# Performance work log

Measured on AMD Instinct MI355X. Metric: run time of the kernel, lower is better.

The kernel has to match this reference:

```python
import jax, jax.numpy as jnp
import numpy as np

B, T, V, D, C, d, TSZ, L, P = 8, 12, 512, 1, 128, 8, 3, 3, 12
BETA = TSZ - 1


def _gauss(emb, mu, isg):
    # Gaussian_component: sum over d of -0.5*(emb-mu)^2 * inv_sigma^2
    return jnp.sum(-0.5 * (emb - mu) ** 2 * isg ** 2, axis=-1)


def _gfs(h, fw, fb, gw, gb):
    # GFS: Conv2d(T->C, kernel (1,C)) over x[B,T,V,C] -> [B,C,V], then 1x1 GLU
    s = jnp.einsum('btvc,otc->bov', h, fw) + fb[None, :, None]
    g = jnp.einsum('bov,po->bpv', s, gw) + gb[None, :, None]
    lhs, rhs = jnp.split(g, 2, axis=1)
    return lhs * jax.nn.sigmoid(rhs)  # B,C,V


def _forward(x, sape, tape, srpe, trpe, zeros_x, zeros_tape, range_mask,
             input_w, input_b, fs0_fc_w, fs0_fc_b, fs0_glu_w, fs0_glu_b,
             mus, inv_sigmas, xproj_w, xproj_b, seproj_w, teproj_w, ln_g, ln_b,
             fs_fc_w, fs_fc_b, fs_glu_w, fs_glu_b, glu_w, glu_b, out_w, out_b):
    h = x @ input_w + input_b  # B,T,V,C (InputLayer)
    tape_pad = jnp.concatenate([zeros_tape, tape], axis=1)  # B,T+beta,1,d
    mask = range_mask.reshape(V, TSZ, V)  # [j, k, i]
    skips = [_gfs(h, fs0_fc_w, fs0_fc_b, fs0_glu_w, fs0_glu_b)]
    for l in range(L):
        h_pad = jnp.concatenate([zeros_x, h], axis=1)  # B,T+beta,V,C
        # all T shifted windows at once (vectorizes the per-timestep loop)
        xwin = jnp.stack([h_pad[:, k:k + T] for k in range(TSZ)], axis=2)     # B,T,k,V,C
        twin = jnp.stack([tape_pad[:, k:k + T] for k in range(TSZ)], axis=2)  # B,T,k,1,d
        mu, isg = mus[l], inv_sigmas[l]
        gi = _gauss(sape, mu[0], isg[0])              # (V,)   source node i
        gj = _gauss(sape, mu[1], isg[1])              # (V,)   target node j
        gti = _gauss(tape, mu[2], isg[2])[:, :, 0]    # (B,T)  tape_i
        gtj = _gauss(twin, mu[3], isg[3])[..., 0]     # (B,T,k) tape_j windows
        ge = _gauss(srpe, mu[4], isg[4])              # (V,V)  [i,j]
        gtr = _gauss(trpe, mu[5], isg[5])[:, 0]       # (k,)
        # log S[b,t,j,k,i]; original gaussian[b,k,i,j] -> reshape -> transpose gives S[b,j,(k,i)]
        logS = (gi[None, None, None, None, :] + gj[None, None, :, None, None]
                + gti[:, :, None, None, None] + gtj[:, :, None, :, None]
                + ge.T[None, None, :, None, :] + gtr[None, None, None, :, None])
        S = jnp.exp(logS) * mask[None, None]          # B,T,V(j),k,V(i)
        # STPGConv: bmm(S, x) over the (k,i) axis
        agg = jnp.einsum('btjki,btkic->btjc', S, xwin)  # B,T,V,C
        z = agg @ xproj_w[l] + xproj_b[l]               # B,T,V,2C
        z = z + sape @ seproj_w[l] + tape @ teproj_w[l]  # SE:(V,2C); TE:(B,T,1,2C) broadcasts over V
        mn = jnp.mean(z, axis=-1, keepdims=True)
        var = jnp.mean((z - mn) ** 2, axis=-1, keepdims=True)
        z = (z - mn) * jax.lax.rsqrt(var + 1e-5) * ln_g[l] + ln_b[l]
        lhs, rhs = jnp.split(z, 2, axis=-1)
        h = lhs * jax.nn.sigmoid(rhs)                   # B,T,V,C
        skips.append(_gfs(h, fs_fc_w[l], fs_fc_b[l], fs_glu_w[l], fs_glu_b[l]))
    hc = jnp.concatenate(skips, axis=1)                 # B,(L+1)*C,V
    g = jnp.einsum('bov,po->bpv', hc, glu_w) + glu_b[None, :, None]
    lhs, rhs = jnp.split(g, 2, axis=1)
    gated = lhs * jax.nn.sigmoid(rhs)                   # B,4C,V
    out = jnp.einsum('bov,po->bpv', gated, out_w) + out_b[None, :, None]  # B,P*D,V
    return out[:, :, :, None]                           # D==1 -> (B,P,V,1)


def setup_inputs() -> dict:
    key = jax.random.key(0)

    def nrm(i, shape, s=1.0):
        return s * jax.random.normal(jax.random.fold_in(key, i), shape, dtype=jnp.float32)

    inp = {
        'x': nrm(0, (B, T, V, D)),
        'sape': nrm(1, (V, d), 0.5),
        'tape': nrm(2, (B, T, 1, d), 0.5),
        'srpe': nrm(3, (V, V, d), 0.5),
        'trpe': nrm(4, (TSZ, 1, d), 0.5),
        'zeros_x': jnp.zeros((B, BETA, V, C), jnp.float32),
        'zeros_tape': jnp.zeros((B, BETA, 1, d), jnp.float32),
        'range_mask': (jax.random.uniform(jax.random.fold_in(key, 5), (V, TSZ * V)) < 0.7).astype(jnp.float32),
        'input_w': nrm(6, (D, C), 0.5),
        'input_b': jnp.zeros((C,), jnp.float32),
        'fs0_fc_w': nrm(7, (C, T, C), 1.0 / np.sqrt(T * C)),
        'fs0_fc_b': jnp.zeros((C,), jnp.float32),
        'fs0_glu_w': nrm(8, (2 * C, C), 1.0 / np.sqrt(C)),
        'fs0_glu_b': jnp.zeros((2 * C,), jnp.float32),
        'mus': nrm(9, (L, 6, d)),
        'inv_sigmas': nrm(10, (L, 6, d), 0.3),
        'xproj_w': nrm(11, (L, C, 2 * C), 1.0 / np.sqrt(C)),
        'xproj_b': jnp.zeros((L, 2 * C), jnp.float32),
        'seproj_w': nrm(12, (L, d, 2 * C), 1.0 / np.sqrt(d)),
        'teproj_w': nrm(13, (L, d, 2 * C), 1.0 / np.sqrt(d)),
        'ln_g': jnp.ones((L, 2 * C), jnp.float32),
        'ln_b': jnp.zeros((L, 2 * C), jnp.float32),
        'fs_fc_w': nrm(14, (L, C, T, C), 1.0 / np.sqrt(T * C)),
        'fs_fc_b': jnp.zeros((L, C), jnp.float32),
        'fs_glu_w': nrm(15, (L, 2 * C, C), 1.0 / np.sqrt(C)),
        'fs_glu_b': jnp.zeros((L, 2 * C), jnp.float32),
        'glu_w': nrm(16, (8 * C, 4 * C), 1.0 / np.sqrt(4 * C)),
        'glu_b': jnp.zeros((8 * C,), jnp.float32),
        'out_w': nrm(17, (P * D, 4 * C), 1.0 / np.sqrt(4 * C)),
        'out_b': jnp.zeros((P * D,), jnp.float32),
    }
    return inp


def reference(x, sape, tape, srpe, trpe, zeros_x, zeros_tape, range_mask,
              input_w, input_b, fs0_fc_w, fs0_fc_b, fs0_glu_w, fs0_glu_b,
              mus, inv_sigmas, xproj_w, xproj_b, seproj_w, teproj_w, ln_g, ln_b,
              fs_fc_w, fs_fc_b, fs_glu_w, fs_glu_b, glu_w, glu_b, out_w, out_b):
    return _forward(x, sape, tape, srpe, trpe, zeros_x, zeros_tape, range_mask,
                    input_w, input_b, fs0_fc_w, fs0_fc_b, fs0_glu_w, fs0_glu_b,
                    mus, inv_sigmas, xproj_w, xproj_b, seproj_w, teproj_w, ln_g, ln_b,
                    fs_fc_w, fs_fc_b, fs_glu_w, fs_glu_b, glu_w, glu_b, out_w, out_b)
```

## Files before the change

kernel.cpp:

```cpp
#include <hip/hip_runtime.h>
#include <cstddef>


#define BB 8
#define TT 12
#define VV 512
#define CC 128

typedef unsigned short ushort_t;
typedef float f32x4 __attribute__((ext_vector_type(4)));
typedef short bf16x8 __attribute__((ext_vector_type(8)));

__device__ __forceinline__ float sigmoidf_(float x){ return 1.0f/(1.0f+expf(-x)); }

__device__ __forceinline__ void split_bf16(float x, ushort_t& hi, ushort_t& lo){
  unsigned u = __float_as_uint(x);
  hi = (ushort_t)(u >> 16);
  float r = x - __uint_as_float(u & 0xFFFF0000u);
  lo = (ushort_t)(__float_as_uint(r) >> 16);
}

__device__ __forceinline__ float gauss8(const float* __restrict__ e,
                                        const float* __restrict__ mu,
                                        const float* __restrict__ sg){
  float a = 0.f;
  #pragma unroll
  for (int dd=0; dd<8; ++dd){
    float df = e[dd]-mu[dd];
    float s  = sg[dd];
    a = fmaf(-0.5f*df*df, s*s, a);
  }
  return a;
}

__global__ __launch_bounds__(256) void k_prep(
    const float* __restrict__ fs0_fc_w, const float* __restrict__ fs_fc_w,
    const float* __restrict__ fs0_glu_w, const float* __restrict__ fs_glu_w,
    const float* __restrict__ glu_w, const float* __restrict__ out_w,
    float* __restrict__ fwT, float* __restrict__ gwT,
    float* __restrict__ gluT, float* __restrict__ outT){
  int job = blockIdx.y;
  int gid = blockIdx.x*256 + threadIdx.x;
  if (job < 4){
    if (gid >= 196608) return;
    const float* src = (job==0) ? fs0_fc_w : fs_fc_w + (size_t)(job-1)*196608;
    float* dst = fwT + (size_t)job*196608;
    int r = gid / 1536, c = gid % 1536;
    dst[(size_t)c*128 + r] = src[gid];
  } else if (job < 8){
    if (gid >= 32768) return;
    int sl = job-4;
    const float* src = (sl==0) ? fs0_glu_w : fs_glu_w + (size_t)(sl-1)*32768;
    float* dst = gwT + (size_t)sl*32768;
    int r = gid / 128, c = gid % 128;
    dst[(size_t)c*256 + r] = src[gid];
  } else if (job == 8){
    if (gid >= 524288) return;
    int r = gid / 512, c = gid % 512;
    gluT[(size_t)c*1024 + r] = glu_w[gid];
  } else {
    if (gid >= 6144) return;
    int r = gid / 512, c = gid % 512;
    outT[(size_t)c*12 + r] = out_w[gid];
  }
}

__global__ __launch_bounds__(256) void k_input(const float* __restrict__ x,
    const float* __restrict__ iw, const float* __restrict__ ib,
    float* __restrict__ hA, ushort_t* __restrict__ hhiT, ushort_t* __restrict__ hloT){
  int bt = blockIdx.x;
  int v0 = blockIdx.y*64;
  int c = threadIdx.x >> 1, half = threadIdx.x & 1;
  int vb = v0 + half*32;
  float wc = iw[c], bc = ib[c];
  const float* xp = x + (size_t)bt*VV + vb;
  float hv[32];
  #pragma unroll
  for (int u=0;u<32;++u) hv[u] = fmaf(xp[u], wc, bc);
  #pragma unroll
  for (int u=0;u<32;++u) hA[((size_t)bt*VV + vb + u)*CC + c] = hv[u];
  unsigned wh[16], wl[16];
  #pragma unroll
  for (int m=0;m<16;++m){
    ushort_t h0,l0,h1,l1;
    split_bf16(hv[2*m],   h0, l0);
    split_bf16(hv[2*m+1], h1, l1);
    wh[m] = (unsigned)h0 | ((unsigned)h1<<16);
    wl[m] = (unsigned)l0 | ((unsigned)l1<<16);
  }
  ushort_t* hp = hhiT + ((size_t)bt*CC + c)*VV + vb;
  ushort_t* lp = hloT + ((size_t)bt*CC + c)*VV + vb;
  #pragma unroll
  for (int q=0;q<4;++q){
    *(uint4*)(hp + q*8) = make_uint4(wh[q*4],wh[q*4+1],wh[q*4+2],wh[q*4+3]);
    *(uint4*)(lp + q*8) = make_uint4(wl[q*4],wl[q*4+1],wl[q*4+2],wl[q*4+3]);
  }
}

__global__ __launch_bounds__(256) void k_gfs1(const float* __restrict__ h,
    const float* __restrict__ fwT, float* __restrict__ s_part){
  int vt = blockIdx.x, b = blockIdx.y, ts = blockIdx.z;
  int tid = threadIdx.x;
  int v0 = vt*32;
  __shared__ float hT[32][34];
  int vtt = tid & 3, ot = tid >> 2;
  float acc[2][8];
  #pragma unroll
  for (int a=0;a<2;++a)
    #pragma unroll
    for (int u=0;u<8;++u) acc[a][u] = 0.f;

  for (int tt=0; tt<3; ++tt){
    int t = ts*3 + tt;
    const float* hbase = h + ((size_t)(b*TT+t)*VV)*CC;
    for (int cch=0; cch<4; ++cch){
      int c0 = cch*32;
      __syncthreads();
      { int vv = tid>>3, c4 = tid&7;
        float4 val = *(const float4*)(hbase + (size_t)(v0+vv)*CC + c0 + c4*4);
        hT[c4*4+0][vv]=val.x; hT[c4*4+1][vv]=val.y;
        hT[c4*4+2][vv]=val.z; hT[c4*4+3][vv]=val.w; }
      __syncthreads();
      const float* fwb = fwT + ((size_t)t*128 + c0)*128 + ot*2;
      for (int c=0;c<32;++c){
        float2 wv = *(const float2*)(fwb + (size_t)c*128);
        float hv[8];
        *(float4*)hv     = *(const float4*)&hT[c][vtt*8];
        *(float4*)(hv+4) = *(const float4*)&hT[c][vtt*8+4];
        #pragma unroll
        for (int u=0;u<8;++u){
          acc[0][u] = fmaf(wv.x, hv[u], acc[0][u]);
          acc[1][u] = fmaf(wv.y, hv[u], acc[1][u]);
        }
      }
    }
  }
  float* sp = s_part + (((size_t)ts*BB+b)*128 + ot*2)*VV + v0 + vtt*8;
  #pragma unroll
  for (int a=0;a<2;++a){
    *(float4*)(sp + (size_t)a*VV)     = *(float4*)&acc[a][0];
    *(float4*)(sp + (size_t)a*VV + 4) = *(float4*)&acc[a][4];
  }
}

__global__ __launch_bounds__(256) void k_gfs2(const float* __restrict__ s_part,
    const float* __restrict__ fb, const float* __restrict__ gwT,
    const float* __restrict__ gb, float* __restrict__ hc, int slot){
  int vt = blockIdx.x, b = blockIdx.y;
  int v0 = vt*32; int tid = threadIdx.x;
  __shared__ float sL[128][36];
  for (int u=0;u<16;++u){
    int lid = u*256 + tid; int o = lid>>5, vv = lid&31;
    float sum = fb[o];
    #pragma unroll
    for (int sp=0;sp<4;++sp)
      sum += s_part[(((size_t)sp*BB+b)*128 + o)*VV + v0 + vv];
    sL[o][vv] = sum;
  }
  __syncthreads();
  int oo = tid & 127, vg = tid >> 7;
  float accL[16], accR[16];
  #pragma unroll
  for (int u=0;u<16;++u){ accL[u]=0.f; accR[u]=0.f; }
  for (int op=0; op<128; ++op){
    float glv = gwT[(size_t)op*256 + oo];
    float grv = gwT[(size_t)op*256 + 128 + oo];
    float sv[16];
    #pragma unroll
    for (int q=0;q<4;++q) *(float4*)(sv+q*4) = *(const float4*)&sL[op][vg*16 + q*4];
    #pragma unroll
    for (int u=0;u<16;++u){ accL[u]=fmaf(glv,sv[u],accL[u]); accR[u]=fmaf(grv,sv[u],accR[u]); }
  }
  float bl = gb[oo], br = gb[128+oo];
  float outv[16];
  #pragma unroll
  for (int u=0;u<16;++u) outv[u] = (accL[u]+bl)*sigmoidf_(accR[u]+br);
  float* dst = hc + ((size_t)b*512 + slot*128 + oo)*VV + v0 + vg*16;
  #pragma unroll
  for (int q=0;q<4;++q) *(float4*)(dst+q*4) = *(float4*)(outv+q*4);
}

__global__ void k_smalls(const float* __restrict__ sape, const float* __restrict__ tape,
    const float* __restrict__ trpe, const float* __restrict__ mus,
    const float* __restrict__ isgs, int l,
    float* __restrict__ gi, float* __restrict__ gj,
    float* __restrict__ E, float* __restrict__ F, float* __restrict__ gtr){
  int tid = threadIdx.x;
  const float* mu = mus  + (size_t)l*48;
  const float* sg = isgs + (size_t)l*48;
  if (tid < 512){
    const float* e = sape + (size_t)tid*8;
    gi[tid] = gauss8(e, mu+0,  sg+0);
    gj[tid] = gauss8(e, mu+8,  sg+8);
  }
  if (tid < 96)
    E[tid] = expf(gauss8(tape + (size_t)tid*8, mu+16, sg+16));
  if (tid < 288){
    int k = tid % 3, bt = tid / 3;
    int t = bt % TT, b = bt / TT;
    int s = t + k - 2;
    F[tid] = (s >= 0) ? expf(gauss8(tape + (size_t)(b*TT+s)*8, mu+24, sg+24)) : 0.f;
  }
  if (tid < 3)
    gtr[tid] = gauss8(trpe + (size_t)tid*8, mu+40, sg+40);
}

__global__ __launch_bounds__(256) void k_W(const float* __restrict__ srpe,
    const float* __restrict__ mask, const float* __restrict__ mus,
    const float* __restrict__ isgs, int l,
    const float* __restrict__ gi, const float* __restrict__ gj,
    const float* __restrict__ gtr,
    ushort_t* __restrict__ Whi, ushort_t* __restrict__ Wlo){
  int it = blockIdx.x, jt = blockIdx.y;
  int tid = threadIdx.x;
  int ii = tid & 15, jj = tid >> 4;
  int i = it*16 + ii, j = jt*16 + jj;
  const float* mu = mus  + (size_t)l*48 + 32;
  const float* sg = isgs + (size_t)l*48 + 32;
  float ge = gauss8(srpe + ((size_t)i*VV + j)*8, mu, sg);
  float base = gi[i] + gj[j] + ge;
  float gk[3] = {gtr[0], gtr[1], gtr[2]};
  __shared__ unsigned tile[16][17];
  int arr = tid>>7, rem = tid&127, jr = rem>>3, p = rem&7;
  for (int k=0;k<3;++k){
    float m = mask[(size_t)j*1536 + k*512 + i];
    float val = m * expf(base + gk[k]);
    ushort_t hi, lo; split_bf16(val, hi, lo);
    __syncthreads();
    tile[jj][ii] = (unsigned)hi | ((unsigned)lo<<16);
    __syncthreads();
    unsigned w0 = tile[jr][2*p], w1 = tile[jr][2*p+1];
    unsigned outw = (arr==0) ? ((w0&0xFFFFu) | (w1<<16))
                             : ((w0>>16) | (w1&0xFFFF0000u));
    ushort_t* dst = (arr ? Wlo : Whi) + ((size_t)k*VV + jt*16 + jr)*VV + it*16 + 2*p;
    *(unsigned*)dst = outw;
  }
}

__global__ __launch_bounds__(256) void k_stpg(
    const ushort_t* __restrict__ hhiT, const ushort_t* __restrict__ hloT,
    const ushort_t* __restrict__ Whi,  const ushort_t* __restrict__ Wlo,
    const float* __restrict__ E, const float* __restrict__ F,
    float* __restrict__ agg){
  int bt = blockIdx.x; int b = bt/TT, t = bt - b*TT;
  int j0 = blockIdx.y * 128;
  int tid = threadIdx.x;
  int lane = tid & 63, wid = tid >> 6;
  int jw = (wid>>1)*64, cw = (wid&1)*64;

  __shared__ ushort_t Ahi_s[128*40];
  __shared__ ushort_t Alo_s[128*40];
  __shared__ ushort_t Bhi_s[128*40];
  __shared__ ushort_t Blo_s[128*40];

  f32x4 acc[4][4];
  #pragma unroll
  for (int a=0;a<4;++a)
    #pragma unroll
    for (int u=0;u<4;++u) acc[a][u] = (f32x4){0.f,0.f,0.f,0.f};

  int kmin = (t>=2) ? 0 : (2-t);
  float Fk[3] = {F[bt*3+0], F[bt*3+1], F[bt*3+2]};
  float Eb = E[bt];

  int ro = (lane&15)*40 + (lane>>4)*8;

  for (int k=kmin; k<3; ++k){
    int s = t + k - 2;
    const ushort_t* gAhi = Whi  + ((size_t)k*VV + j0)*VV;
    const ushort_t* gAlo = Wlo  + ((size_t)k*VV + j0)*VV;
    const ushort_t* gBhi = hhiT + (size_t)(b*TT+s)*CC*VV;
    const ushort_t* gBlo = hloT + (size_t)(b*TT+s)*CC*VV;
    for (int i0=0; i0<512; i0+=32){
      __syncthreads();
      #pragma unroll
      for (int p=0;p<2;++p){
        int sl = p*256 + tid;
        int r = sl>>2, q = sl&3;
        size_t go = (size_t)r*VV + i0 + q*8;
        int lo_ = r*40 + q*8;
        *(uint4*)&Ahi_s[lo_] = *(const uint4*)(gAhi + go);
        *(uint4*)&Alo_s[lo_] = *(const uint4*)(gAlo + go);
        *(uint4*)&Bhi_s[lo_] = *(const uint4*)(gBhi + go);
        *(uint4*)&Blo_s[lo_] = *(const uint4*)(gBlo + go);
      }
      __syncthreads();
      bf16x8 ah[4], al[4], bh[4], bl[4];
      #pragma unroll
      for (int f=0; f<4; ++f){
        ah[f] = *(const bf16x8*)&Ahi_s[(jw + f*16)*40 + ro];
        al[f] = *(const bf16x8*)&Alo_s[(jw + f*16)*40 + ro];
        bh[f] = *(const bf16x8*)&Bhi_s[(cw + f*16)*40 + ro];
        bl[f] = *(const bf16x8*)&Blo_s[(cw + f*16)*40 + ro];
      }
      #pragma unroll
      for (int jf=0;jf<4;++jf)
        #pragma unroll
        for (int cf=0;cf<4;++cf){
          acc[jf][cf] = __builtin_amdgcn_mfma_f32_16x16x32_bf16(ah[jf], bh[cf], acc[jf][cf],0,0,0);
          acc[jf][cf] = __builtin_amdgcn_mfma_f32_16x16x32_bf16(ah[jf], bl[cf], acc[jf][cf],0,0,0);
          acc[jf][cf] = __builtin_amdgcn_mfma_f32_16x16x32_bf16(al[jf], bh[cf], acc[jf][cf],0,0,0);
        }
    }
    if (k < 2){
      float r = Fk[k]/Fk[k+1];
      #pragma unroll
      for (int jf=0;jf<4;++jf)
        #pragma unroll
        for (int cf=0;cf<4;++cf) acc[jf][cf] *= r;
    }
  }
  float fin = Fk[2]*Eb;
  #pragma unroll
  for (int jf=0;jf<4;++jf){
    #pragma unroll
    for (int cf=0;cf<4;++cf){
      int row = j0 + jw + jf*16 + (lane>>4)*4;
      int col = cw + cf*16 + (lane&15);
      float* dst = agg + ((size_t)bt*VV + row)*CC + col;
      #pragma unroll
      for (int e=0;e<4;++e) dst[(size_t)e*CC] = acc[jf][cf][e]*fin;
    }
  }
}

__global__ __launch_bounds__(256) void k_xln(float* __restrict__ hB,
    const float* __restrict__ xw, const float* __restrict__ xb,
    const float* __restrict__ sw, const float* __restrict__ tw,
    const float* __restrict__ sape, const float* __restrict__ tape,
    const float* __restrict__ lng, const float* __restrict__ lnb, int l,
    ushort_t* __restrict__ hhiT, ushort_t* __restrict__ hloT){
  int v0 = blockIdx.x * 8;
  int bt = blockIdx.y;
  int tid = threadIdx.x;
  __shared__ float aL[8][128];
  __shared__ float se[8][8];
  __shared__ float te[8];
  __shared__ float zL[8][260];
  __shared__ float stat[8][2];
  float* hrow = hB + ((size_t)bt*VV + v0)*CC;
  { int vv = tid>>5, cc4 = tid&31;
    *(float4*)&aL[vv][cc4*4] = *(const float4*)(hrow + (size_t)vv*CC + cc4*4); }
  if (tid < 64) se[tid>>3][tid&7] = sape[(size_t)(v0 + (tid>>3))*8 + (tid&7)];
  if (tid >= 64 && tid < 72) te[tid-64] = tape[(size_t)bt*8 + (tid-64)];
  __syncthreads();

  const float* xwl = xw + (size_t)l*32768;
  const float* swl = sw + (size_t)l*2048;
  const float* twl = tw + (size_t)l*2048;
  float common = xb[l*256 + tid];
  #pragma unroll
  for (int dd=0; dd<8; ++dd) common = fmaf(te[dd], twl[dd*256+tid], common);
  float z[8];
  #pragma unroll
  for (int vv=0; vv<8; ++vv){
    float sacc = common;
    #pragma unroll
    for (int dd=0; dd<8; ++dd) sacc = fmaf(se[vv][dd], swl[dd*256+tid], sacc);
    z[vv] = sacc;
  }
  for (int c4=0; c4<32; ++c4){
    float x0 = xwl[(c4*4+0)*256 + tid];
    float x1 = xwl[(c4*4+1)*256 + tid];
    float x2 = xwl[(c4*4+2)*256 + tid];
    float x3 = xwl[(c4*4+3)*256 + tid];
    #pragma unroll
    for (int vv=0; vv<8; ++vv){
      float4 a4 = *(const float4*)&aL[vv][c4*4];
      z[vv] = fmaf(a4.x,x0, fmaf(a4.y,x1, fmaf(a4.z,x2, fmaf(a4.w,x3, z[vv]))));
    }
  }
  #pragma unroll
  for (int vv=0; vv<8; ++vv) zL[vv][tid] = z[vv];
  __syncthreads();
  { int vv = tid>>5, sub = tid&31;
    float s1=0.f, s2=0.f;
    #pragma unroll
    for (int u=0; u<8; ++u){ float val = zL[vv][sub + u*32]; s1 += val; s2 = fmaf(val,val,s2); }
    #pragma unroll
    for (int off=16; off>=1; off>>=1){
      s1 += __shfl_down(s1, off, 32);
      s2 += __shfl_down(s2, off, 32);
    }
    if (sub==0){
      float mn = s1*(1.f/256.f);
      float var = s2*(1.f/256.f) - mn*mn;
      stat[vv][0] = mn;
      stat[vv][1] = 1.f/sqrtf(var + 1e-5f);
    }
  }
  __syncthreads();
  { int vv = tid>>5, sub = tid&31;
    float mn = stat[vv][0], rs = stat[vv][1];
    float4 zl = *(const float4*)&zL[vv][sub*4];
    float4 zr = *(const float4*)&zL[vv][sub*4+128];
    float zlv[4] = {zl.x,zl.y,zl.z,zl.w};
    float zrv[4] = {zr.x,zr.y,zr.z,zr.w};
    float ov[4];
    #pragma unroll
    for (int u=0; u<4; ++u){
      int c = sub*4 + u;
      float nl = (zlv[u]-mn)*rs*lng[l*256 + c]       + lnb[l*256 + c];
      float nr = (zrv[u]-mn)*rs*lng[l*256 + 128 + c] + lnb[l*256 + 128 + c];
      ov[u] = nl * sigmoidf_(nr);
    }
    *(float4*)(hrow + (size_t)vv*CC + sub*4) = *(float4*)ov;
    zL[vv][sub*4+0]=ov[0]; zL[vv][sub*4+1]=ov[1]; zL[vv][sub*4+2]=ov[2]; zL[vv][sub*4+3]=ov[3];
  }
  __syncthreads();
  { int cc = tid & 127, sel = tid >> 7;
    float g[8];
    #pragma unroll
    for (int u=0;u<8;++u) g[u] = zL[u][cc];
    unsigned w[4];
    #pragma unroll
    for (int m=0;m<4;++m){
      ushort_t h0,l0,h1,l1;
      split_bf16(g[2*m],   h0, l0);
      split_bf16(g[2*m+1], h1, l1);
      w[m] = sel ? ((unsigned)l0 | ((unsigned)l1<<16))
                 : ((unsigned)h0 | ((unsigned)h1<<16));
    }
    ushort_t* dst = (sel ? hloT : hhiT) + ((size_t)bt*CC + cc)*VV + v0;
    *(uint4*)dst = make_uint4(w[0],w[1],w[2],w[3]);
  }
}

__global__ __launch_bounds__(256) void k_final(const float* __restrict__ hc,
    const float* __restrict__ gluT, const float* __restrict__ glub,
    const float* __restrict__ outT, const float* __restrict__ outb,
    float* __restrict__ out){
  int b = blockIdx.y; int v0 = blockIdx.x * 8;
  int tid = threadIdx.x;
  __shared__ float hcl[512][8];
  __shared__ float gl[512][9];
  for (int u=0; u<16; ++u){
    int lid = u*256 + tid; int o = lid>>3, vv = lid&7;
    hcl[o][vv] = hc[((size_t)b*512 + o)*VV + v0 + vv];
  }
  __syncthreads();
  float aL0[8], aR0[8], aL1[8], aR1[8];
  #pragma unroll
  for (int u=0;u<8;++u){ aL0[u]=0.f; aR0[u]=0.f; aL1[u]=0.f; aR1[u]=0.f; }
  for (int o=0; o<512; ++o){
    const float* grow = gluT + (size_t)o*1024;
    float g0 = grow[tid], g1 = grow[tid+256], g2 = grow[tid+512], g3 = grow[tid+768];
    float hv[8];
    *(float4*)hv     = *(const float4*)&hcl[o][0];
    *(float4*)(hv+4) = *(const float4*)&hcl[o][4];
    #pragma unroll
    for (int u=0;u<8;++u){
      aL0[u]=fmaf(g0,hv[u],aL0[u]); aL1[u]=fmaf(g1,hv[u],aL1[u]);
      aR0[u]=fmaf(g2,hv[u],aR0[u]); aR1[u]=fmaf(g3,hv[u],aR1[u]);
    }
  }
  float bL0 = glub[tid], bL1 = glub[tid+256], bR0 = glub[tid+512], bR1 = glub[tid+768];
  #pragma unroll
  for (int u=0;u<8;++u){
    gl[tid][u]     = (aL0[u]+bL0)*sigmoidf_(aR0[u]+bR0);
    gl[tid+256][u] = (aL1[u]+bL1)*sigmoidf_(aR1[u]+bR1);
  }
  __syncthreads();
  if (tid < 96){
    int r = tid>>3, vv = tid&7;
    float acc = outb[r];
    for (int q=0; q<512; ++q) acc = fmaf(outT[(size_t)q*12 + r], gl[q][vv], acc);
    out[(size_t)b*6144 + r*512 + v0 + vv] = acc;
  }
}

extern "C" void kernel_launch(void* const* d_in, const int* in_sizes, int n_in,
                              void* d_out, int out_size, void* d_ws, size_t ws_size,
                              hipStream_t stream){
  const float* x        = (const float*)d_in[0];
  const float* sape     = (const float*)d_in[1];
  const float* tape     = (const float*)d_in[2];
  const float* srpe     = (const float*)d_in[3];
  const float* trpe     = (const float*)d_in[4];
  const float* mask     = (const float*)d_in[7];
  const float* input_w  = (const float*)d_in[8];
  const float* input_b  = (const float*)d_in[9];
  const float* fs0_fc_w = (const float*)d_in[10];
  const float* fs0_fc_b = (const float*)d_in[11];
  const float* fs0_glu_w= (const float*)d_in[12];
  const float* fs0_glu_b= (const float*)d_in[13];
  const float* mus      = (const float*)d_in[14];
  const float* isg      = (const float*)d_in[15];
  const float* xproj_w  = (const float*)d_in[16];
  const float* xproj_b  = (const float*)d_in[17];
  const float* seproj_w = (const float*)d_in[18];
  const float* teproj_w = (const float*)d_in[19];
  const float* ln_g     = (const float*)d_in[20];
  const float* ln_b     = (const float*)d_in[21];
  const float* fs_fc_w  = (const float*)d_in[22];
  const float* fs_fc_b  = (const float*)d_in[23];
  const float* fs_glu_w = (const float*)d_in[24];
  const float* fs_glu_b = (const float*)d_in[25];
  const float* glu_w    = (const float*)d_in[26];
  const float* glu_b    = (const float*)d_in[27];
  const float* out_w    = (const float*)d_in[28];
  const float* out_b    = (const float*)d_in[29];

  float* ws    = (float*)d_ws;
  float* hA    = ws;
  float* hc    = hA    + 6291456;
  float* s_part= hc    + 2097152;
  float* fwT   = s_part+ 2097152;
  float* gwT   = fwT   + 786432;
  float* gluT  = gwT   + 131072;
  float* outT  = gluT  + 524288;
  float* gi    = outT  + 6144;
  float* gj    = gi    + 512;
  float* Ebuf  = gj    + 512;
  float* Fbuf  = Ebuf  + 96;
  float* gtr   = Fbuf  + 288;
  ushort_t* hhiT = (ushort_t*)(gtr + 16);
  ushort_t* hloT = hhiT + 6291456;
  ushort_t* Whi  = hloT + 6291456;
  ushort_t* Wlo  = Whi  + 786432;

  k_prep<<<dim3(2048,10),256,0,stream>>>(fs0_fc_w, fs_fc_w, fs0_glu_w, fs_glu_w,
                                         glu_w, out_w, fwT, gwT, gluT, outT);
  k_input<<<dim3(96,8),256,0,stream>>>(x, input_w, input_b, hA, hhiT, hloT);
  k_gfs1<<<dim3(16,8,4),256,0,stream>>>(hA, fwT, s_part);
  k_gfs2<<<dim3(16,8),256,0,stream>>>(s_part, fs0_fc_b, gwT, fs0_glu_b, hc, 0);

  for (int l=0; l<3; ++l){
    k_smalls<<<1,512,0,stream>>>(sape, tape, trpe, mus, isg, l, gi, gj, Ebuf, Fbuf, gtr);
    k_W<<<dim3(32,32),256,0,stream>>>(srpe, mask, mus, isg, l, gi, gj, gtr, Whi, Wlo);
    k_stpg<<<dim3(96,4),256,0,stream>>>(hhiT, hloT, Whi, Wlo, Ebuf, Fbuf, hA);
    k_xln<<<dim3(64,96),256,0,stream>>>(hA, xproj_w, xproj_b, seproj_w, teproj_w,
                                        sape, tape, ln_g, ln_b, l, hhiT, hloT);
    k_gfs1<<<dim3(16,8,4),256,0,stream>>>(hA, fwT + (size_t)(l+1)*196608, s_part);
    k_gfs2<<<dim3(16,8),256,0,stream>>>(s_part, fs_fc_b + l*128, gwT + (size_t)(l+1)*32768,
                                        fs_glu_b + l*256, hc, l+1);
  }
  k_final<<<dim3(64,8),256,0,stream>>>(hc, gluT, glu_b, outT, out_b, (float*)d_out);
}
```

Before: 992.8 us.

## Rewrite projection+LayerNorm+GLU kernel on bf16x3 MFMA with concatenated weights

The per-layer x/spatial/temporal projection kernel, previously a scalar FP32 FMA loop over 8 nodes per block, now runs on MFMA 16x16x32 bf16 instructions with a hi/lo split (three products) to keep near-FP32 accuracy. The projection, spatial and temporal embedding weights plus the bias are packed once in the prep kernel into a single K=160 concatenated matrix. The embeddings and a constant-one column are folded into the A operand. LayerNorm statistics are reduced across lanes with shuffles, and each block now covers 128 nodes. This targets the compute-bound scalar GEMM, at the cost of heavy register use (32 accumulators) and only 384 blocks.

```diff
diff --git a/kernel.cpp b/kernel.cpp
--- a/kernel.cpp
+++ b/kernel.cpp
@@ -37,8 +37,11 @@
     const float* __restrict__ fs0_fc_w, const float* __restrict__ fs_fc_w,
     const float* __restrict__ fs0_glu_w, const float* __restrict__ fs_glu_w,
     const float* __restrict__ glu_w, const float* __restrict__ out_w,
+    const float* __restrict__ xw, const float* __restrict__ sw,
+    const float* __restrict__ tw, const float* __restrict__ xb2,
     float* __restrict__ fwT, float* __restrict__ gwT,
-    float* __restrict__ gluT, float* __restrict__ outT){
+    float* __restrict__ gluT, float* __restrict__ outT,
+    ushort_t* __restrict__ xcat_hi, ushort_t* __restrict__ xcat_lo){
   int job = blockIdx.y;
   int gid = blockIdx.x*256 + threadIdx.x;
   if (job < 4){
@@ -58,10 +61,25 @@
     if (gid >= 524288) return;
     int r = gid / 512, c = gid % 512;
     gluT[(size_t)c*1024 + r] = glu_w[gid];
-  } else {
+  } else if (job == 9){
     if (gid >= 6144) return;
     int r = gid / 512, c = gid % 512;
     outT[(size_t)c*12 + r] = out_w[gid];
+  } else {
+    if (gid >= 122880) return;
+    int ll  = gid / 40960;
+    int rem = gid - ll*40960;
+    int col = rem / 160;
+    int k   = rem - col*160;
+    float val;
+    if (k < 128)       val = xw[(size_t)ll*32768 + (size_t)k*256 + col];
+    else if (k < 136)  val = sw[(size_t)ll*2048 + (size_t)(k-128)*256 + col];
+    else if (k < 144)  val = tw[(size_t)ll*2048 + (size_t)(k-136)*256 + col];
+    else if (k == 144) val = xb2[ll*256 + col];
+    else               val = 0.f;
+    ushort_t hi, lo; split_bf16(val, hi, lo);
+    xcat_hi[gid] = hi;
+    xcat_lo[gid] = lo;
   }
 }
 
@@ -324,105 +342,127 @@
   }
 }
 
-__global__ __launch_bounds__(256) void k_xln(float* __restrict__ hB,
-    const float* __restrict__ xw, const float* __restrict__ xb,
-    const float* __restrict__ sw, const float* __restrict__ tw,
+__global__ __launch_bounds__(256,2) void k_xln2(
+    float* __restrict__ hA,
+    const ushort_t* __restrict__ xcat_hi, const ushort_t* __restrict__ xcat_lo,
     const float* __restrict__ sape, const float* __restrict__ tape,
     const float* __restrict__ lng, const float* __restrict__ lnb, int l,
     ushort_t* __restrict__ hhiT, ushort_t* __restrict__ hloT){
-  int v0 = blockIdx.x * 8;
-  int bt = blockIdx.y;
+  int vt = blockIdx.x, bt = blockIdx.y;
+  int v0 = vt*128;
   int tid = threadIdx.x;
-  __shared__ float aL[8][128];
-  __shared__ float se[8][8];
-  __shared__ float te[8];
-  __shared__ float zL[8][260];
-  __shared__ float stat[8][2];
-  float* hrow = hB + ((size_t)bt*VV + v0)*CC;
-  { int vv = tid>>5, cc4 = tid&31;
-    *(float4*)&aL[vv][cc4*4] = *(const float4*)(hrow + (size_t)vv*CC + cc4*4); }
-  if (tid < 64) se[tid>>3][tid&7] = sape[(size_t)(v0 + (tid>>3))*8 + (tid&7)];
-  if (tid >= 64 && tid < 72) te[tid-64] = tape[(size_t)bt*8 + (tid-64)];
+  int lane = tid & 63, w = tid >> 6;
+  int l15 = lane & 15, l4 = lane >> 4;
+  int ko = l4*8;
+
+  __shared__ float sef[128][8];
+  __shared__ float tef[8];
+  __shared__ float lnwS[256], lnbS[256];
+  { int r2 = tid>>1, hh = tid&1;
+    *(float4*)&sef[r2][hh*4] = *(const float4*)(sape + (size_t)(v0+r2)*8 + hh*4); }
+  if (tid < 8) tef[tid] = tape[(size_t)bt*8 + tid];
+  lnwS[tid] = lng[l*256 + tid];
+  lnbS[tid] = lnb[l*256 + tid];
   __syncthreads();
 
-  const float* xwl = xw + (size_t)l*32768;
-  const float* swl = sw + (size_t)l*2048;
-  const float* twl = tw + (size_t)l*2048;
-  float common = xb[l*256 + tid];
-  #pragma unroll
-  for (int dd=0; dd<8; ++dd) common = fmaf(te[dd], twl[dd*256+tid], common);
-  float z[8];
-  #pragma unroll
-  for (int vv=0; vv<8; ++vv){
-    float sacc = common;
-    #pragma unroll
-    for (int dd=0; dd<8; ++dd) sacc = fmaf(se[vv][dd], swl[dd*256+tid], sacc);
-    z[vv] = sacc;
-  }
-  for (int c4=0; c4<32; ++c4){
-    float x0 = xwl[(c4*4+0)*256 + tid];
-    float x1 = xwl[(c4*4+1)*256 + tid];
-    float x2 = xwl[(c4*4+2)*256 + tid];
-    float x3 = xwl[(c4*4+3)*256 + tid];
-    #pragma unroll
-    for (int vv=0; vv<8; ++vv){
-      float4 a4 = *(const float4*)&aL[vv][c4*4];
-      z[vv] = fmaf(a4.x,x0, fmaf(a4.y,x1, fmaf(a4.z,x2, fmaf(a4.w,x3, z[vv]))));
-    }
-  }
-  #pragma unroll
-  for (int vv=0; vv<8; ++vv) zL[vv][tid] = z[vv];
-  __syncthreads();
-  { int vv = tid>>5, sub = tid&31;
-    float s1=0.f, s2=0.f;
-    #pragma unroll
-    for (int u=0; u<8; ++u){ float val = zL[vv][sub + u*32]; s1 += val; s2 = fmaf(val,val,s2); }
-    #pragma unroll
-    for (int off=16; off>=1; off>>=1){
-      s1 += __shfl_down(s1, off, 32);
-      s2 += __shfl_down(s2, off, 32);
-    }
-    if (sub==0){
-      float mn = s1*(1.f/256.f);
-      float var = s2*(1.f/256.f) - mn*mn;
-      stat[vv][0] = mn;
-      stat[vv][1] = 1.f/sqrtf(var + 1e-5f);
-    }
-  }
-  __syncthreads();
-  { int vv = tid>>5, sub = tid&31;
-    float mn = stat[vv][0], rs = stat[vv][1];
-    float4 zl = *(const float4*)&zL[vv][sub*4];
-    float4 zr = *(const float4*)&zL[vv][sub*4+128];
-    float zlv[4] = {zl.x,zl.y,zl.z,zl.w};
-    float zrv[4] = {zr.x,zr.y,zr.z,zr.w};
-    float ov[4];
-    #pragma unroll
-    for (int u=0; u<4; ++u){
-      int c = sub*4 + u;
-      float nl = (zlv[u]-mn)*rs*lng[l*256 + c]       + lnb[l*256 + c];
-      float nr = (zrv[u]-mn)*rs*lng[l*256 + 128 + c] + lnb[l*256 + 128 + c];
-      ov[u] = nl * sigmoidf_(nr);
-    }
-    *(float4*)(hrow + (size_t)vv*CC + sub*4) = *(float4*)ov;
-    zL[vv][sub*4+0]=ov[0]; zL[vv][sub*4+1]=ov[1]; zL[vv][sub*4+2]=ov[2]; zL[vv][sub*4+3]=ov[3];
-  }
-  __syncthreads();
-  { int cc = tid & 127, sel = tid >> 7;
-    float g[8];
-    #pragma unroll
-    for (int u=0;u<8;++u) g[u] = zL[u][cc];
-    unsigned w[4];
-    #pragma unroll
-    for (int m=0;m<4;++m){
-      ushort_t h0,l0,h1,l1;
-      split_bf16(g[2*m],   h0, l0);
-      split_bf16(g[2*m+1], h1, l1);
-      w[m] = sel ? ((unsigned)l0 | ((unsigned)l1<<16))
-                 : ((unsigned)h0 | ((unsigned)h1<<16));
-    }
-    ushort_t* dst = (sel ? hloT : hhiT) + ((size_t)bt*CC + cc)*VV + v0;
-    *(uint4*)dst = make_uint4(w[0],w[1],w[2],w[3]);
+  f32x4 acc[2][16];
+  #pragma unroll
+  for (int m=0;m<2;++m)
+    #pragma unroll
+    for (int n=0;n<16;++n) acc[m][n] = (f32x4){0.f,0.f,0.f,0.f};
+
+  const ushort_t* bhb = xcat_hi + (size_t)l*40960;
+  const ushort_t* blb = xcat_lo + (size_t)l*40960;
+
+  #pragma unroll
+  for (int ks=0; ks<5; ++ks){
+    bf16x8 a_h[2], a_l[2];
+    #pragma unroll
+    for (int m=0;m<2;++m){
+      int lrow = w*32 + m*16 + l15;
+      float av[8];
+      if (ks < 4){
+        const float* ap = hA + ((size_t)bt*VV + v0 + lrow)*CC + ks*32 + ko;
+        *(float4*)av     = *(const float4*)ap;
+        *(float4*)(av+4) = *(const float4*)(ap+4);
+      } else {
+        #pragma unroll
+        for (int u=0;u<8;++u) av[u] = 0.f;
+        if (l4==0){
+          #pragma unroll
+          for (int u=0;u<8;++u) av[u] = sef[lrow][u];
+        } else if (l4==1){
+          #pragma unroll
+          for (int u=0;u<8;++u) av[u] = tef[u];
+        } else if (l4==2){
+          av[0] = 1.f;
+        }
+      }
+      #pragma unroll
+      for (int u=0;u<8;++u){
+        ushort_t hi, lo; split_bf16(av[u], hi, lo);
+        a_h[m][u] = (short)hi; a_l[m][u] = (short)lo;
+      }
+    }
+    #pragma unroll
+    for (int n=0;n<16;++n){
+      size_t boff = (size_t)(n*16 + l15)*160 + ks*32 + ko;
+      bf16x8 b_h = *(const bf16x8*)(bhb + boff);
+      bf16x8 b_l = *(const bf16x8*)(blb + boff);
+      #pragma unroll
+      for (int m=0;m<2;++m){
+        acc[m][n] = __builtin_amdgcn_mfma_f32_16x16x32_bf16(a_h[m], b_h, acc[m][n],0,0,0);
+        acc[m][n] = __builtin_amdgcn_mfma_f32_16x16x32_bf16(a_h[m], b_l, acc[m][n],0,0,0);
+        acc[m][n] = __builtin_amdgcn_mfma_f32_16x16x32_bf16(a_l[m], b_h, acc[m][n],0,0,0);
+      }
+    }
+  }
+
+  float mn[2][4], rs[2][4];
+  #pragma unroll
+  for (int m=0;m<2;++m){
+    #pragma unroll
+    for (int e=0;e<4;++e){
+      float s1=0.f, s2=0.f;
+      #pragma unroll
+      for (int n=0;n<16;++n){ float v = acc[m][n][e]; s1 += v; s2 = fmaf(v,v,s2); }
+      #pragma unroll
+      for (int off=8; off>=1; off>>=1){
+        s1 += __shfl_xor(s1, off, 64);
+        s2 += __shfl_xor(s2, off, 64);
+      }
+      float mu = s1*(1.f/256.f);
+      mn[m][e] = mu;
+      rs[m][e] = 1.f/sqrtf(s2*(1.f/256.f) - mu*mu + 1e-5f);
+    }
+  }
+
+  float* hbase = hA + ((size_t)bt*VV)*CC;
+  #pragma unroll
+  for (int m=0;m<2;++m){
+    #pragma unroll
+    for (int n=0;n<8;++n){
+      int cL = n*16 + l15, cR = cL + 128;
+      float gL = lnwS[cL], bL = lnbS[cL];
+      float gR = lnwS[cR], bR = lnbS[cR];
+      ushort_t hi4[4], lo4[4];
+      #pragma unroll
+      for (int e=0;e<4;++e){
+        float nl = (acc[m][n][e]   - mn[m][e])*rs[m][e]*gL + bL;
+        float nr = (acc[m][n+8][e] - mn[m][e])*rs[m][e]*gR + bR;
+        float hv = nl * sigmoidf_(nr);
+        int v = v0 + w*32 + m*16 + l4*4 + e;
+        hbase[(size_t)v*CC + cL] = hv;
+        split_bf16(hv, hi4[e], lo4[e]);
+      }
+      int vbase = v0 + w*32 + m*16 + l4*4;
+      ushort_t* hp = hhiT + ((size_t)bt*CC + cL)*VV + vbase;
+      ushort_t* lp = hloT + ((size_t)bt*CC + cL)*VV + vbase;
+      *(uint2*)hp = make_uint2((unsigned)hi4[0] | ((unsigned)hi4[1]<<16),
+                               (unsigned)hi4[2] | ((unsigned)hi4[3]<<16));
+      *(uint2*)lp = make_uint2((unsigned)lo4[0] | ((unsigned)lo4[1]<<16),
+                               (unsigned)lo4[2] | ((unsigned)lo4[3]<<16));
+    }
   }
 }
 
@@ -518,9 +558,13 @@
   ushort_t* hloT = hhiT + 6291456;
   ushort_t* Whi  = hloT + 6291456;
   ushort_t* Wlo  = Whi  + 786432;
-
-  k_prep<<<dim3(2048,10),256,0,stream>>>(fs0_fc_w, fs_fc_w, fs0_glu_w, fs_glu_w,
-                                         glu_w, out_w, fwT, gwT, gluT, outT);
+  ushort_t* xcat_hi = Wlo + 786432;
+  ushort_t* xcat_lo = xcat_hi + 122880;
+
+  k_prep<<<dim3(2048,11),256,0,stream>>>(fs0_fc_w, fs_fc_w, fs0_glu_w, fs_glu_w,
+                                         glu_w, out_w, xproj_w, seproj_w, teproj_w,
+                                         xproj_b, fwT, gwT, gluT, outT,
+                                         xcat_hi, xcat_lo);
   k_input<<<dim3(96,8),256,0,stream>>>(x, input_w, input_b, hA, hhiT, hloT);
   k_gfs1<<<dim3(16,8,4),256,0,stream>>>(hA, fwT, s_part);
   k_gfs2<<<dim3(16,8),256,0,stream>>>(s_part, fs0_fc_b, gwT, fs0_glu_b, hc, 0);
@@ -529,8 +573,8 @@
     k_smalls<<<1,512,0,stream>>>(sape, tape, trpe, mus, isg, l, gi, gj, Ebuf, Fbuf, gtr);
     k_W<<<dim3(32,32),256,0,stream>>>(srpe, mask, mus, isg, l, gi, gj, gtr, Whi, Wlo);
     k_stpg<<<dim3(96,4),256,0,stream>>>(hhiT, hloT, Whi, Wlo, Ebuf, Fbuf, hA);
-    k_xln<<<dim3(64,96),256,0,stream>>>(hA, xproj_w, xproj_b, seproj_w, teproj_w,
-                                        sape, tape, ln_g, ln_b, l, hhiT, hloT);
+    k_xln2<<<dim3(4,96),256,0,stream>>>(hA, xcat_hi, xcat_lo, sape, tape,
+                                        ln_g, ln_b, l, hhiT, hloT);
     k_gfs1<<<dim3(16,8,4),256,0,stream>>>(hA, fwT + (size_t)(l+1)*196608, s_part);
     k_gfs2<<<dim3(16,8),256,0,stream>>>(s_part, fs_fc_b + l*128, gwT + (size_t)(l+1)*32768,
                                         fs_glu_b + l*256, hc, l+1);
```

New measurement: 877.6 us. 11.6% less time.
